# Optimization experiments

Measured on AMD Instinct MI355X. Metric: run time of the kernel, lower is better.

The kernel has to match this reference:

```python
import jax, jax.numpy as jnp
import numpy as np

D = 512          # token_dim * num_heads
TOKEN_DIM = 256
SCALE = TOKEN_DIM ** (-0.5)


def _l2norm(x, axis):
    # torch.nn.functional.normalize: x / max(||x||_2, eps)
    n = jnp.linalg.norm(x, axis=axis, keepdims=True)
    return x / jnp.maximum(n, 1e-12)


def setup_inputs() -> dict:
    key = jax.random.key(0)
    ks = jax.random.split(key, 32)
    B, N, IN = 8, 4096, 512
    s_in = 1.0 / np.sqrt(IN)
    s_d = 1.0 / np.sqrt(D)

    def lin(k, fin, fout, scale):
        kw, kb = jax.random.split(k)
        return (jax.random.uniform(kw, (fin, fout), jnp.float32, -scale, scale),
                jax.random.uniform(kb, (fout,), jnp.float32, -scale, scale))

    wq_I, bq_I = lin(ks[0], IN, D, s_in)
    wk_I, bk_I = lin(ks[1], IN, D, s_in)
    wq_M, bq_M = lin(ks[2], IN, D, s_in)
    wk_M, bk_M = lin(ks[3], IN, D, s_in)
    p1_w, p1_b = lin(ks[4], D, D, s_d)
    p2_w, p2_b = lin(ks[5], D, D, s_d)
    p3_w, p3_b = lin(ks[6], D, D, s_d)
    p4_w, p4_b = lin(ks[7], D, D, s_d)
    f_w, f_b = lin(ks[8], D, TOKEN_DIM, s_d)
    return {
        'x_I': jax.random.normal(ks[9], (B, N, IN), jnp.float32),
        'x_M': jax.random.normal(ks[10], (B, N, IN), jnp.float32),
        'wq_I': wq_I, 'bq_I': bq_I, 'wk_I': wk_I, 'bk_I': bk_I,
        'wq_M': wq_M, 'bq_M': bq_M, 'wk_M': wk_M, 'bk_M': bk_M,
        'wg_I': jax.random.normal(ks[11], (D, 1), jnp.float32),
        'wg_M': jax.random.normal(ks[12], (D, 1), jnp.float32),
        'p1_w': p1_w, 'p1_b': p1_b, 'p2_w': p2_w, 'p2_b': p2_b,
        'p3_w': p3_w, 'p3_b': p3_b, 'p4_w': p4_w, 'p4_b': p4_b,
        'f_w': f_w, 'f_b': f_b,
    }


def reference(x_I, x_M, wq_I, bq_I, wk_I, bk_I, wq_M, bq_M, wk_M, bk_M,
              wg_I, wg_M, p1_w, p1_b, p2_w, p2_b, p3_w, p3_b, p4_w, p4_b,
              f_w, f_b):
    # projections, then L2-normalize along feature dim
    q_I = _l2norm(x_I @ wq_I + bq_I, axis=-1)   # [B, N, D]
    k_I = _l2norm(x_I @ wk_I + bk_I, axis=-1)
    q_M = _l2norm(x_M @ wq_M + bq_M, axis=-1)
    k_M = _l2norm(x_M @ wk_M + bk_M, axis=-1)

    # softmax-free attention weights, L2-normalized over sequence dim
    A_I = _l2norm((q_I @ wg_I) * SCALE, axis=1)  # [B, N, 1]
    A_M = _l2norm((q_M @ wg_M) * SCALE, axis=1)

    # pooled global queries, broadcast back over tokens
    G_I = jnp.sum(A_I * q_I, axis=1, keepdims=True)  # [B, 1, D]
    G_M = jnp.sum(A_M * q_M, axis=1, keepdims=True)

    out = ((G_I * k_I) @ p1_w + p1_b
           + (G_I * k_M) @ p2_w + p2_b
           + (G_M * k_M) @ p3_w + p3_b
           + (G_M * k_I) @ p4_w + p4_b
           + q_I + q_M)                              # [B, N, D]
    return out @ f_w + f_b                           # [B, N, token_dim]
```

## Files before the change

kernel.cpp:

```cpp
#include <hip/hip_runtime.h>

typedef unsigned short u16;
typedef unsigned int   u32;
typedef __bf16 bf16_t;
typedef bf16_t bf16x8 __attribute__((ext_vector_type(8)));
typedef float  f32x4  __attribute__((ext_vector_type(4)));

__device__ __forceinline__ float b2f(u16 u){
  u32 x = ((u32)u) << 16;
  return __builtin_bit_cast(float, x);
}
__device__ __forceinline__ u16 f2b(float f){
  u32 u = __builtin_bit_cast(u32, f);
  u32 r = u + 0x7FFFu + ((u >> 16) & 1u);
  return (u16)(r >> 16);
}

union V8 { uint4 q; u16 u[8]; };

__device__ __forceinline__ void gld16(const u16* gsrc, u16* ldst){
  __builtin_amdgcn_global_load_lds(
      (const __attribute__((address_space(1))) u32*)gsrc,
      (__attribute__((address_space(3))) u32*)ldst, 16, 0, 0);
}

struct CArgs { const float* src[4]; u16* dst[4]; int cnt[4]; };

__global__ __launch_bounds__(256) void convert_k(CArgs c){
  int z = blockIdx.z;
  int i8 = (blockIdx.x * 256 + threadIdx.x) * 8;
  if (i8 >= c.cnt[z]) return;
  const float* s = c.src[z] + i8;
  float4 a = *(const float4*)s;
  float4 b = *(const float4*)(s + 4);
  V8 o;
  o.u[0]=f2b(a.x); o.u[1]=f2b(a.y); o.u[2]=f2b(a.z); o.u[3]=f2b(a.w);
  o.u[4]=f2b(b.x); o.u[5]=f2b(b.y); o.u[6]=f2b(b.z); o.u[7]=f2b(b.w);
  *(uint4*)(c.dst[z] + i8) = o.q;
}

struct TArgs { const float* src[5]; u16* dst[5]; int ncol[5]; };

__global__ __launch_bounds__(256) void transpose_k(TArgs t,
    const float* __restrict__ p1b, const float* __restrict__ p2b,
    const float* __restrict__ p3b, const float* __restrict__ p4b,
    const float* __restrict__ fw, const float* __restrict__ fb,
    float* __restrict__ cb, float* __restrict__ Gun)
{
  __shared__ u16 T[64][65];
  __shared__ float sb[512];
  int z = blockIdx.z;
  int tid = threadIdx.x;
  if (z == 5){
    if (blockIdx.x == 0 && blockIdx.y == 0){
      sb[tid]       = p1b[tid] + p2b[tid] + p3b[tid] + p4b[tid];
      sb[tid + 256] = p1b[tid+256] + p2b[tid+256] + p3b[tid+256] + p4b[tid+256];
      __syncthreads();
      float acc = 0.f;
      for (int j = 0; j < 512; j++) acc += sb[j] * fw[j*256 + tid];
      cb[tid] = acc + fb[tid];
    } else if (blockIdx.x >= 1 && blockIdx.x <= 4){
      int idx = ((blockIdx.x - 1)*8 + blockIdx.y)*256 + tid;
      Gun[idx] = 0.f;
    }
    return;
  }
  int nc = t.ncol[z];
  int j0 = blockIdx.y * 64;
  if (j0 >= nc) return;
  int i0 = blockIdx.x * 64;
  const float* s = t.src[z];
  u16* d = t.dst[z];
  #pragma unroll
  for (int rep = 0; rep < 16; rep++){
    int lin = rep*256 + tid;
    int r = lin >> 6, c = lin & 63;
    T[c][r] = f2b(s[(size_t)(i0 + r) * nc + j0 + c]);
  }
  __syncthreads();
  #pragma unroll
  for (int rep = 0; rep < 16; rep++){
    int lin = rep*256 + tid;
    int r = lin >> 6, c = lin & 63;
    d[(size_t)(j0 + r) * 512 + i0 + c] = T[r][c];
  }
}

__global__ __launch_bounds__(256, 2) void proj_k(
    const float* __restrict__ XI, const float* __restrict__ XM,
    const u16* __restrict__ WTI, const u16* __restrict__ WTM,
    const float* __restrict__ bqI, const float* __restrict__ bkI,
    const float* __restrict__ bqM, const float* __restrict__ bkM,
    const float* __restrict__ wgI, const float* __restrict__ wgM,
    u16* __restrict__ qI, u16* __restrict__ kI,
    u16* __restrict__ qM, u16* __restrict__ kM,
    float* __restrict__ Araw, float* __restrict__ Gun)
{
  const int tid = threadIdx.x, l = tid & 63, w = tid >> 6;
  const int m0 = blockIdx.x * 64;
  const int y  = blockIdx.y, zi = blockIdx.z;
  __shared__ __align__(16) u16 As[64*32];
  __shared__ __align__(16) u16 Bs[512*32];
  const int lr = l & 15, quad = l >> 4;
  const int srow = l >> 2, scol = (l & 3) * 8;
  const int wn = w * 128;

  const float* X  = zi ? XM : XI;
  const u16* Wbase = (zi ? WTM : WTI) + (size_t)y * 512 * 512;
  const float* bias = y ? (zi ? bkM : bkI) : (zi ? bqM : bqI);
  const float* wg   = zi ? wgM : wgI;
  u16* OUT = y ? (zi ? kM : kI) : (zi ? qM : qI);

  const int arow = w*16 + (l >> 2);
  const int aks  = (l & 3) * 8;

  f32x4 acc[4][8] = {};
  for (int k0 = 0; k0 < 512; k0 += 32){
    __syncthreads();
    {
      const float* src = X + (size_t)(m0 + arow)*512 + k0 + aks;
      float4 p0 = *(const float4*)src;
      float4 p1 = *(const float4*)(src + 4);
      V8 o;
      o.u[0]=f2b(p0.x); o.u[1]=f2b(p0.y); o.u[2]=f2b(p0.z); o.u[3]=f2b(p0.w);
      o.u[4]=f2b(p1.x); o.u[5]=f2b(p1.y); o.u[6]=f2b(p1.z); o.u[7]=f2b(p1.w);
      *(uint4*)&As[arow*32 + aks] = o.q;
    }
    #pragma unroll
    for (int i = 0; i < 8; i++)
      gld16(Wbase + (size_t)(wn + i*16 + srow)*512 + k0 + scol, &Bs[(w*8 + i)*512]);
    __syncthreads();
    bf16x8 aF[4], bF[8];
    #pragma unroll
    for (int mt = 0; mt < 4; mt++)
      aF[mt] = *(const bf16x8*)&As[(mt*16 + lr)*32 + quad*8];
    #pragma unroll
    for (int nt = 0; nt < 8; nt++)
      bF[nt] = *(const bf16x8*)&Bs[(wn + nt*16 + lr)*32 + quad*8];
    #pragma unroll
    for (int mt = 0; mt < 4; mt++){
      #pragma unroll
      for (int nt = 0; nt < 8; nt++)
        acc[mt][nt] = __builtin_amdgcn_mfma_f32_16x16x32_bf16(aF[mt], bF[nt], acc[mt][nt], 0, 0, 0);
    }
  }

  float wgv[8];
  if (y == 0){
    #pragma unroll
    for (int nt = 0; nt < 8; nt++) wgv[nt] = wg[wn + nt*16 + lr];
  }
  #pragma unroll
  for (int nt = 0; nt < 8; nt++){
    float bcol = bias[wn + nt*16 + lr];
    #pragma unroll
    for (int mt = 0; mt < 4; mt++)
      #pragma unroll
      for (int r = 0; r < 4; r++)
        acc[mt][nt][r] += bcol;
  }
  float ss[4][4], dq[4][4];
  #pragma unroll
  for (int mt = 0; mt < 4; mt++)
    #pragma unroll
    for (int r = 0; r < 4; r++){
      float s = 0.f, d = 0.f;
      #pragma unroll
      for (int nt = 0; nt < 8; nt++){
        float v = acc[mt][nt][r];
        s += v*v;
        if (y == 0) d += v * wgv[nt];
      }
      ss[mt][r] = s; dq[mt][r] = d;
    }
  #pragma unroll
  for (int off = 1; off < 16; off <<= 1){
    #pragma unroll
    for (int mt = 0; mt < 4; mt++)
      #pragma unroll
      for (int r = 0; r < 4; r++){
        ss[mt][r] += __shfl_xor(ss[mt][r], off, 64);
        if (y == 0) dq[mt][r] += __shfl_xor(dq[mt][r], off, 64);
      }
  }
  __syncthreads();
  float* red    = (float*)As;
  float* red2   = red + 256;
  float* rnS    = red2 + 256;
  float* araw_s = rnS + 64;
  if (lr == 0){
    #pragma unroll
    for (int mt = 0; mt < 4; mt++)
      #pragma unroll
      for (int r = 0; r < 4; r++){
        int row = mt*16 + quad*4 + r;
        red[w*64 + row] = ss[mt][r];
        if (y == 0) red2[w*64 + row] = dq[mt][r];
      }
  }
  __syncthreads();
  if (tid < 64){
    float t2 = red[tid] + red[64+tid] + red[128+tid] + red[192+tid];
    float rn = 1.f / fmaxf(sqrtf(t2), 1e-12f);
    rnS[tid] = rn;
    if (y == 0){
      float d = red2[tid] + red2[64+tid] + red2[128+tid] + red2[192+tid];
      float a = d * rn * 0.0625f;
      araw_s[tid] = a;
      Araw[zi*32768 + m0 + tid] = a;
    }
  }
  __syncthreads();
  float part[8] = {};
  #pragma unroll
  for (int mt = 0; mt < 4; mt++){
    f32x4 rn4 = *(const f32x4*)&rnS[mt*16 + quad*4];
    #pragma unroll
    for (int r = 0; r < 4; r++){
      float aw = (y == 0) ? araw_s[mt*16 + quad*4 + r] : 0.f;
      #pragma unroll
      for (int nt = 0; nt < 8; nt++){
        float v = acc[mt][nt][r] * rn4[r];
        OUT[(size_t)(m0 + mt*16 + quad*4 + r)*512 + wn + nt*16 + lr] = f2b(v);
        if (y == 0) part[nt] += aw * v;
      }
    }
  }
  if (y == 0){
    #pragma unroll
    for (int nt = 0; nt < 8; nt++){
      part[nt] += __shfl_xor(part[nt], 16, 64);
      part[nt] += __shfl_xor(part[nt], 32, 64);
    }
    if (quad == 0){
      int bb = blockIdx.x >> 6;
      #pragma unroll
      for (int nt = 0; nt < 8; nt++)
        atomicAdd(&Gun[((size_t)zi*8 + bb)*512 + wn + nt*16 + lr], part[nt]);
    }
  }
}

template<int MODE>
__global__ __launch_bounds__(256) void gemm2_k(
    const u16* __restrict__ A0, const u16* __restrict__ A1,
    const u16* __restrict__ A2, const u16* __restrict__ A3,
    const u16* __restrict__ BT,
    const float* __restrict__ cb,
    u16* __restrict__ Cq, float* __restrict__ Cf)
{
  constexpr int KTOT = (MODE == 2) ? 2048 : 512;
  const int tid = threadIdx.x, l = tid & 63, w = tid >> 6;
  const int m0 = blockIdx.x * 128, n0 = blockIdx.y * 128;
  __shared__ u16 As[128*32];
  __shared__ u16 Bs[128*32];
  f32x4 acc[4][4] = {};
  const int wm = (w >> 1) * 64, wn = (w & 1) * 64;
  const int lr = l & 15, quad = l >> 4;
  const int srow = l >> 2, scol = (l & 3) * 8;

  const u16* Bbase = BT;
  u16* Cqb = Cq;
  if constexpr (MODE == 2)
    Bbase = BT + (size_t)(m0 >> 12) * 256 * 2048;
  if constexpr (MODE == 1){
    Bbase = BT + (size_t)blockIdx.z * 262144;
    Cqb   = Cq + (size_t)blockIdx.z * 131072;
  }

  for (int k0 = 0; k0 < KTOT; k0 += 32){
    __syncthreads();
    const u16* Ab; int kloc;
    if constexpr (MODE == 2){
      int which = k0 >> 9; kloc = k0 & 511;
      Ab = (which == 0) ? A0 : (which == 1) ? A1 : (which == 2) ? A2 : A3;
    } else { Ab = A0; kloc = k0; }
    #pragma unroll
    for (int i = 0; i < 2; i++){
      int r = w*32 + i*16 + srow;
      gld16(Ab    + (size_t)(m0 + r) * 512  + kloc + scol, &As[(w*2 + i) * 512]);
      gld16(Bbase + (size_t)(n0 + r) * KTOT + k0   + scol, &Bs[(w*2 + i) * 512]);
    }
    __syncthreads();
    bf16x8 aF[4], bF[4];
    #pragma unroll
    for (int mt = 0; mt < 4; mt++)
      aF[mt] = *(const bf16x8*)&As[(wm + mt*16 + lr)*32 + quad*8];
    #pragma unroll
    for (int nt = 0; nt < 4; nt++)
      bF[nt] = *(const bf16x8*)&Bs[(wn + nt*16 + lr)*32 + quad*8];
    #pragma unroll
    for (int mt = 0; mt < 4; mt++){
      #pragma unroll
      for (int nt = 0; nt < 4; nt++)
        acc[mt][nt] = __builtin_amdgcn_mfma_f32_16x16x32_bf16(aF[mt], bF[nt], acc[mt][nt], 0, 0, 0);
    }
  }
  #pragma unroll
  for (int nt = 0; nt < 4; nt++){
    int col = n0 + wn + nt*16 + lr;
    #pragma unroll
    for (int mt = 0; mt < 4; mt++){
      int row0 = m0 + wm + mt*16 + quad*4;
      #pragma unroll
      for (int r = 0; r < 4; r++){
        int row = row0 + r;
        float v = acc[mt][nt][r];
        if constexpr (MODE == 1){
          Cqb[(size_t)row*512 + col] = f2b(v);
        } else {
          Cf[(size_t)row*256 + col] = v + cb[col];
        }
      }
    }
  }
}

__global__ __launch_bounds__(256) void ranorm_k(const float* __restrict__ Araw,
                                                float* __restrict__ rA){
  int idx = blockIdx.x;
  const float* A = Araw + idx*4096;
  int tid = threadIdx.x, l = tid & 63, w = tid >> 6;
  float ss = 0.f;
  for (int i = tid; i < 4096; i += 256){ float a = A[i]; ss += a*a; }
  #pragma unroll
  for (int off = 32; off > 0; off >>= 1) ss += __shfl_xor(ss, off, 64);
  __shared__ float red[4];
  if (l == 0) red[w] = ss;
  __syncthreads();
  if (tid == 0)
    rA[idx] = 1.f / fmaxf(sqrtf(red[0] + red[1] + red[2] + red[3]), 1e-12f);
}

__global__ __launch_bounds__(256) void weff_k(
    const u16* __restrict__ pfT, const u16* __restrict__ fT,
    const float* __restrict__ Gun, const float* __restrict__ rA,
    u16* __restrict__ WT)
{
  int b = blockIdx.x, o = blockIdx.y, tid = threadIdx.x;
  int k0 = tid * 8;
  V8 out;
  if (k0 < 1024){
    int kk = k0 & 511;
    const u16* pa = pfT + ((k0 < 512) ? 0      : 131072) + o*512 + kk;
    const u16* pb = pfT + ((k0 < 512) ? 393216 : 262144) + o*512 + kk;
    float rI = rA[b], rM = rA[8 + b];
    const float* gI = Gun + b*512 + kk;
    const float* gM = Gun + 4096 + b*512 + kk;
    V8 Pa, Pb; Pa.q = *(const uint4*)pa; Pb.q = *(const uint4*)pb;
    float4 gi0 = *(const float4*)gI, gi1 = *(const float4*)(gI+4);
    float4 gm0 = *(const float4*)gM, gm1 = *(const float4*)(gM+4);
    float gi[8] = {gi0.x,gi0.y,gi0.z,gi0.w,gi1.x,gi1.y,gi1.z,gi1.w};
    float gm[8] = {gm0.x,gm0.y,gm0.z,gm0.w,gm1.x,gm1.y,gm1.z,gm1.w};
    #pragma unroll
    for (int j = 0; j < 8; j++)
      out.u[j] = f2b(rI*gi[j]*b2f(Pa.u[j]) + rM*gm[j]*b2f(Pb.u[j]));
  } else {
    out.q = *(const uint4*)(fT + o*512 + (k0 & 511));
  }
  *(uint4*)(WT + ((size_t)b*256 + o)*2048 + k0) = out.q;
}

extern "C" void kernel_launch(void* const* d_in, const int* in_sizes, int n_in,
                              void* d_out, int out_size, void* d_ws, size_t ws_size,
                              hipStream_t stream)
{
  const float* x_I  = (const float*)d_in[0];
  const float* x_M  = (const float*)d_in[1];
  const float* wq_I = (const float*)d_in[2];
  const float* bq_I = (const float*)d_in[3];
  const float* wk_I = (const float*)d_in[4];
  const float* bk_I = (const float*)d_in[5];
  const float* wq_M = (const float*)d_in[6];
  const float* bq_M = (const float*)d_in[7];
  const float* wk_M = (const float*)d_in[8];
  const float* bk_M = (const float*)d_in[9];
  const float* wg_I = (const float*)d_in[10];
  const float* wg_M = (const float*)d_in[11];
  const float* p1_w = (const float*)d_in[12];
  const float* p1_b = (const float*)d_in[13];
  const float* p2_w = (const float*)d_in[14];
  const float* p2_b = (const float*)d_in[15];
  const float* p3_w = (const float*)d_in[16];
  const float* p3_b = (const float*)d_in[17];
  const float* p4_w = (const float*)d_in[18];
  const float* p4_b = (const float*)d_in[19];
  const float* f_w  = (const float*)d_in[20];
  const float* f_b  = (const float*)d_in[21];

  char* ws = (char*)d_ws;
  u16*  wqkT_I = (u16*)(ws + 0);
  u16*  wqkT_M = (u16*)(ws + 1048576);
  u16*  fT     = (u16*)(ws + 2097152);
  u16*  pcat   = (u16*)(ws + 2359296);
  u16*  pfT    = (u16*)(ws + 4456448);
  u16*  WT     = (u16*)(ws + 5505024);
  float* cb    = (float*)(ws + 13893632);
  float* Araw  = (float*)(ws + 13894656);
  float* rA    = (float*)(ws + 14156800);
  float* Gun   = (float*)(ws + 14157056);
  u16*  qIb    = (u16*)(ws + 14189824);
  u16*  kIb    = (u16*)(ws + 47744256);
  u16*  qMb    = (u16*)(ws + 81298688);
  u16*  kMb    = (u16*)(ws + 114853120);

  CArgs c;
  const float* csrc[4] = {p1_w, p2_w, p3_w, p4_w};
  u16* cdst[4] = {pcat, pcat + 262144, pcat + 524288, pcat + 786432};
  for (int i = 0; i < 4; i++){ c.src[i] = csrc[i]; c.dst[i] = cdst[i]; c.cnt[i] = 262144; }
  convert_k<<<dim3(128,1,4), 256, 0, stream>>>(c);

  TArgs t;
  const float* tsrc[5] = {wq_I, wk_I, wq_M, wk_M, f_w};
  u16* tdst[5] = {wqkT_I, wqkT_I + 262144, wqkT_M, wqkT_M + 262144, fT};
  int tnc[5] = {512, 512, 512, 512, 256};
  for (int i = 0; i < 5; i++){ t.src[i] = tsrc[i]; t.dst[i] = tdst[i]; t.ncol[i] = tnc[i]; }
  transpose_k<<<dim3(8,8,6), 256, 0, stream>>>(t, p1_b, p2_b, p3_b, p4_b, f_w, f_b, cb, Gun);

  gemm2_k<1><<<dim3(2,4,4), 256, 0, stream>>>(fT, nullptr, nullptr, nullptr,
      pcat, nullptr, pfT, nullptr);

  proj_k<<<dim3(512,2,2), 256, 0, stream>>>(x_I, x_M, wqkT_I, wqkT_M,
      bq_I, bk_I, bq_M, bk_M, wg_I, wg_M, qIb, kIb, qMb, kMb, Araw, Gun);

  ranorm_k<<<16, 256, 0, stream>>>(Araw, rA);

  weff_k<<<dim3(8,256), 256, 0, stream>>>(pfT, fT, Gun, rA, WT);

  gemm2_k<2><<<dim3(256,2), 256, 0, stream>>>(kIb, kMb, qIb, qMb,
      WT, cb, nullptr, (float*)d_out);
}
```

Baseline: 399.7 us.

## Double-buffer LDS tiles in projection and GEMM kernels to overlap loads

Both the projection kernel and the templated GEMM kernel now keep two LDS buffers for the A and B tiles. The loads for the next K-step are issued before the MFMA work on the current step, and only one barrier per iteration remains. In the projection kernel the fp32 activations are loaded early and converted to bf16 after the MFMAs, hiding global latency. This doubles LDS use: the projection kernel goes to about 72KB per block at a target of 2 blocks per CU, which may pressure occupancy and raise register use.

After: 392.2 us. Within noise of the previous version (-1.9%).

```diff
diff --git a/kernel.cpp b/kernel.cpp
--- a/kernel.cpp
+++ b/kernel.cpp
@@ -99,8 +99,8 @@
   const int tid = threadIdx.x, l = tid & 63, w = tid >> 6;
   const int m0 = blockIdx.x * 64;
   const int y  = blockIdx.y, zi = blockIdx.z;
-  __shared__ __align__(16) u16 As[64*32];
-  __shared__ __align__(16) u16 Bs[512*32];
+  __shared__ __align__(16) u16 As[2][64*32];
+  __shared__ __align__(16) u16 Bs[2][512*32];
   const int lr = l & 15, quad = l >> 4;
   const int srow = l >> 2, scol = (l & 3) * 8;
   const int wn = w * 128;
@@ -113,36 +113,56 @@
 
   const int arow = w*16 + (l >> 2);
   const int aks  = (l & 3) * 8;
+  const float* aptr = X + (size_t)(m0 + arow)*512 + aks;
 
   f32x4 acc[4][8] = {};
-  for (int k0 = 0; k0 < 512; k0 += 32){
-    __syncthreads();
-    {
-      const float* src = X + (size_t)(m0 + arow)*512 + k0 + aks;
-      float4 p0 = *(const float4*)src;
-      float4 p1 = *(const float4*)(src + 4);
+
+  {
+    float4 p0 = *(const float4*)(aptr);
+    float4 p1 = *(const float4*)(aptr + 4);
+    V8 o;
+    o.u[0]=f2b(p0.x); o.u[1]=f2b(p0.y); o.u[2]=f2b(p0.z); o.u[3]=f2b(p0.w);
+    o.u[4]=f2b(p1.x); o.u[5]=f2b(p1.y); o.u[6]=f2b(p1.z); o.u[7]=f2b(p1.w);
+    *(uint4*)&As[0][arow*32 + aks] = o.q;
+    #pragma unroll
+    for (int i = 0; i < 8; i++)
+      gld16(Wbase + (size_t)(wn + i*16 + srow)*512 + scol, &Bs[0][(w*8 + i)*512]);
+  }
+  __syncthreads();
+
+  #pragma unroll
+  for (int kk = 0; kk < 16; kk++){
+    const int k0 = kk * 32;
+    const int cur = kk & 1, nxt = cur ^ 1;
+    const int kn = k0 + 32;
+    float4 p0, p1;
+    if (kn < 512){
+      #pragma unroll
+      for (int i = 0; i < 8; i++)
+        gld16(Wbase + (size_t)(wn + i*16 + srow)*512 + kn + scol, &Bs[nxt][(w*8 + i)*512]);
+      p0 = *(const float4*)(aptr + kn);
+      p1 = *(const float4*)(aptr + kn + 4);
+    }
+    bf16x8 aF[4], bF[8];
+    #pragma unroll
+    for (int mt = 0; mt < 4; mt++)
+      aF[mt] = *(const bf16x8*)&As[cur][(mt*16 + lr)*32 + quad*8];
+    #pragma unroll
+    for (int nt = 0; nt < 8; nt++)
+      bF[nt] = *(const bf16x8*)&Bs[cur][(wn + nt*16 + lr)*32 + quad*8];
+    #pragma unroll
+    for (int mt = 0; mt < 4; mt++){
+      #pragma unroll
+      for (int nt = 0; nt < 8; nt++)
+        acc[mt][nt] = __builtin_amdgcn_mfma_f32_16x16x32_bf16(aF[mt], bF[nt], acc[mt][nt], 0, 0, 0);
+    }
+    if (kn < 512){
       V8 o;
       o.u[0]=f2b(p0.x); o.u[1]=f2b(p0.y); o.u[2]=f2b(p0.z); o.u[3]=f2b(p0.w);
       o.u[4]=f2b(p1.x); o.u[5]=f2b(p1.y); o.u[6]=f2b(p1.z); o.u[7]=f2b(p1.w);
-      *(uint4*)&As[arow*32 + aks] = o.q;
-    }
-    #pragma unroll
-    for (int i = 0; i < 8; i++)
-      gld16(Wbase + (size_t)(wn + i*16 + srow)*512 + k0 + scol, &Bs[(w*8 + i)*512]);
+      *(uint4*)&As[nxt][arow*32 + aks] = o.q;
+    }
     __syncthreads();
-    bf16x8 aF[4], bF[8];
-    #pragma unroll
-    for (int mt = 0; mt < 4; mt++)
-      aF[mt] = *(const bf16x8*)&As[(mt*16 + lr)*32 + quad*8];
-    #pragma unroll
-    for (int nt = 0; nt < 8; nt++)
-      bF[nt] = *(const bf16x8*)&Bs[(wn + nt*16 + lr)*32 + quad*8];
-    #pragma unroll
-    for (int mt = 0; mt < 4; mt++){
-      #pragma unroll
-      for (int nt = 0; nt < 8; nt++)
-        acc[mt][nt] = __builtin_amdgcn_mfma_f32_16x16x32_bf16(aF[mt], bF[nt], acc[mt][nt], 0, 0, 0);
-    }
   }
 
   float wgv[8];
@@ -252,8 +272,8 @@
   constexpr int KTOT = (MODE == 2) ? 2048 : 512;
   const int tid = threadIdx.x, l = tid & 63, w = tid >> 6;
   const int m0 = blockIdx.x * 128, n0 = blockIdx.y * 128;
-  __shared__ u16 As[128*32];
-  __shared__ u16 Bs[128*32];
+  __shared__ u16 As[2][128*32];
+  __shared__ u16 Bs[2][128*32];
   f32x4 acc[4][4] = {};
   const int wm = (w >> 1) * 64, wn = (w & 1) * 64;
   const int lr = l & 15, quad = l >> 4;
@@ -268,34 +288,47 @@
     Cqb   = Cq + (size_t)blockIdx.z * 131072;
   }
 
+  #pragma unroll
+  for (int i = 0; i < 2; i++){
+    int r = w*32 + i*16 + srow;
+    gld16(A0    + (size_t)(m0 + r) * 512  + scol, &As[0][(w*2 + i) * 512]);
+    gld16(Bbase + (size_t)(n0 + r) * KTOT + scol, &Bs[0][(w*2 + i) * 512]);
+  }
+  __syncthreads();
+
+  #pragma unroll 2
   for (int k0 = 0; k0 < KTOT; k0 += 32){
-    __syncthreads();
-    const u16* Ab; int kloc;
-    if constexpr (MODE == 2){
-      int which = k0 >> 9; kloc = k0 & 511;
-      Ab = (which == 0) ? A0 : (which == 1) ? A1 : (which == 2) ? A2 : A3;
-    } else { Ab = A0; kloc = k0; }
-    #pragma unroll
-    for (int i = 0; i < 2; i++){
-      int r = w*32 + i*16 + srow;
-      gld16(Ab    + (size_t)(m0 + r) * 512  + kloc + scol, &As[(w*2 + i) * 512]);
-      gld16(Bbase + (size_t)(n0 + r) * KTOT + k0   + scol, &Bs[(w*2 + i) * 512]);
-    }
-    __syncthreads();
+    const int cur = (k0 >> 5) & 1, nxt = cur ^ 1;
+    const int kn = k0 + 32;
+    if (kn < KTOT){
+      const u16* Ab; int kloc;
+      if constexpr (MODE == 2){
+        int which = kn >> 9; kloc = kn & 511;
+        Ab = (which == 0) ? A0 : (which == 1) ? A1 : (which == 2) ? A2 : A3;
+      } else { Ab = A0; kloc = kn; }
+      #pragma unroll
+      for (int i = 0; i < 2; i++){
+        int r = w*32 + i*16 + srow;
+        gld16(Ab    + (size_t)(m0 + r) * 512  + kloc + scol, &As[nxt][(w*2 + i) * 512]);
+        gld16(Bbase + (size_t)(n0 + r) * KTOT + kn   + scol, &Bs[nxt][(w*2 + i) * 512]);
+      }
+    }
     bf16x8 aF[4], bF[4];
     #pragma unroll
     for (int mt = 0; mt < 4; mt++)
-      aF[mt] = *(const bf16x8*)&As[(wm + mt*16 + lr)*32 + quad*8];
+      aF[mt] = *(const bf16x8*)&As[cur][(wm + mt*16 + lr)*32 + quad*8];
     #pragma unroll
     for (int nt = 0; nt < 4; nt++)
-      bF[nt] = *(const bf16x8*)&Bs[(wn + nt*16 + lr)*32 + quad*8];
+      bF[nt] = *(const bf16x8*)&Bs[cur][(wn + nt*16 + lr)*32 + quad*8];
     #pragma unroll
     for (int mt = 0; mt < 4; mt++){
       #pragma unroll
       for (int nt = 0; nt < 4; nt++)
         acc[mt][nt] = __builtin_amdgcn_mfma_f32_16x16x32_bf16(aF[mt], bF[nt], acc[mt][nt], 0, 0, 0);
     }
-  }
+    __syncthreads();
+  }
+
   #pragma unroll
   for (int nt = 0; nt < 4; nt++){
     int col = n0 + wn + nt*16 + lr;
```

## Software-pipeline projection and second-stage GEMMs with multi-buffered LDS prefetch

Applied to the files above, without the earlier changes.

The projection kernel now double-buffers both the bf16-converted activation tile and the weight tile. Global loads for the next K-step are issued before the MFMAs of the current step, and the previous two syncthreads per iteration become a single barrier guarded by explicit vmcnt waits. The second GEMM kernel gets a 4-deep LDS ring with three stages in flight, setprio around the MFMA block, and launch bounds of 2 blocks per SM. This is meant to hide global-load latency behind compute, at the cost of more LDS per block, which may limit occupancy. The hand-written waitcnt and barrier sequencing also makes correctness fragile.

New measurement: 386.4 us. 1.03x faster.

```diff
diff --git a/kernel.cpp b/kernel.cpp
--- a/kernel.cpp
+++ b/kernel.cpp
@@ -99,51 +99,105 @@
   const int tid = threadIdx.x, l = tid & 63, w = tid >> 6;
   const int m0 = blockIdx.x * 64;
   const int y  = blockIdx.y, zi = blockIdx.z;
-  __shared__ __align__(16) u16 As[64*32];
-  __shared__ __align__(16) u16 Bs[512*32];
+  __shared__ __align__(16) u16 As[2][64*32];
+  __shared__ __align__(16) u16 Bs[2][4][4096];
   const int lr = l & 15, quad = l >> 4;
   const int srow = l >> 2, scol = (l & 3) * 8;
   const int wn = w * 128;
 
   const float* X  = zi ? XM : XI;
-  const u16* Wbase = (zi ? WTM : WTI) + (size_t)y * 512 * 512;
+  const u16* Wbase = (zi ? WTM : WTI) + (size_t)y * 512 * 512 + (size_t)wn * 512;
   const float* bias = y ? (zi ? bkM : bkI) : (zi ? bqM : bqI);
   const float* wg   = zi ? wgM : wgI;
   u16* OUT = y ? (zi ? kM : kI) : (zi ? qM : qI);
 
   const int arow = w*16 + (l >> 2);
   const int aks  = (l & 3) * 8;
+  const float* aptr = X + (size_t)(m0 + arow)*512 + aks;
 
   f32x4 acc[4][8] = {};
-  for (int k0 = 0; k0 < 512; k0 += 32){
-    __syncthreads();
-    {
-      const float* src = X + (size_t)(m0 + arow)*512 + k0 + aks;
-      float4 p0 = *(const float4*)src;
-      float4 p1 = *(const float4*)(src + 4);
-      V8 o;
-      o.u[0]=f2b(p0.x); o.u[1]=f2b(p0.y); o.u[2]=f2b(p0.z); o.u[3]=f2b(p0.w);
-      o.u[4]=f2b(p1.x); o.u[5]=f2b(p1.y); o.u[6]=f2b(p1.z); o.u[7]=f2b(p1.w);
-      *(uint4*)&As[arow*32 + aks] = o.q;
-    }
-    #pragma unroll
-    for (int i = 0; i < 8; i++)
-      gld16(Wbase + (size_t)(wn + i*16 + srow)*512 + k0 + scol, &Bs[(w*8 + i)*512]);
-    __syncthreads();
+  float4 s0a, s0b, s1a, s1b;
+
+  s0a = *(const float4*)(aptr);
+  s0b = *(const float4*)(aptr + 4);
+  __builtin_amdgcn_sched_barrier(0);
+  #pragma unroll
+  for (int i = 0; i < 8; i++)
+    gld16(Wbase + (size_t)(i*16 + srow)*512 + scol, &Bs[0][w][i*512]);
+  __builtin_amdgcn_sched_barrier(0);
+  s1a = *(const float4*)(aptr + 32);
+  s1b = *(const float4*)(aptr + 36);
+  __builtin_amdgcn_sched_barrier(0);
+  {
+    V8 o;
+    o.u[0]=f2b(s0a.x); o.u[1]=f2b(s0a.y); o.u[2]=f2b(s0a.z); o.u[3]=f2b(s0a.w);
+    o.u[4]=f2b(s0b.x); o.u[5]=f2b(s0b.y); o.u[6]=f2b(s0b.z); o.u[7]=f2b(s0b.w);
+    *(uint4*)&As[0][arow*32 + aks] = o.q;
+  }
+  asm volatile("s_waitcnt vmcnt(2)" ::: "memory");
+  asm volatile("s_waitcnt lgkmcnt(0)" ::: "memory");
+  __builtin_amdgcn_sched_barrier(0);
+  __builtin_amdgcn_s_barrier();
+
+#define PBODY(P, CV0, CV1, LD0, LD1, KA, KB, DOLOAD, VMC) do{                              \
+    bf16x8 aF[4], bF[8];                                                                   \
+    _Pragma("unroll")                                                                      \
+    for (int mt = 0; mt < 4; mt++)                                                         \
+      aF[mt] = *(const bf16x8*)&As[(P)][(mt*16 + lr)*32 + quad*8];                         \
+    _Pragma("unroll")                                                                      \
+    for (int nt = 0; nt < 8; nt++)                                                         \
+      bF[nt] = *(const bf16x8*)&Bs[(P)][w][(nt*16 + lr)*32 + quad*8];                      \
+    __builtin_amdgcn_sched_barrier(0);                                                     \
+    _Pragma("unroll")                                                                      \
+    for (int i = 0; i < 8; i++)                                                            \
+      gld16(Wbase + (size_t)(i*16 + srow)*512 + (KB) + scol, &Bs[(P)^1][w][i*512]);        \
+    __builtin_amdgcn_sched_barrier(0);                                                     \
+    if (DOLOAD){                                                                           \
+      LD0 = *(const float4*)(aptr + (KA));                                                 \
+      LD1 = *(const float4*)(aptr + (KA) + 4);                                             \
+    }                                                                                      \
+    __builtin_amdgcn_sched_barrier(0);                                                     \
+    { V8 o;                                                                                \
+      o.u[0]=f2b((CV0).x); o.u[1]=f2b((CV0).y); o.u[2]=f2b((CV0).z); o.u[3]=f2b((CV0).w); \
+      o.u[4]=f2b((CV1).x); o.u[5]=f2b((CV1).y); o.u[6]=f2b((CV1).z); o.u[7]=f2b((CV1).w); \
+      *(uint4*)&As[(P)^1][arow*32 + aks] = o.q; }                                          \
+    __builtin_amdgcn_s_setprio(1);                                                         \
+    _Pragma("unroll")                                                                      \
+    for (int mt = 0; mt < 4; mt++){                                                        \
+      _Pragma("unroll")                                                                    \
+      for (int nt = 0; nt < 8; nt++)                                                       \
+        acc[mt][nt] = __builtin_amdgcn_mfma_f32_16x16x32_bf16(aF[mt], bF[nt], acc[mt][nt], 0, 0, 0); \
+    }                                                                                      \
+    __builtin_amdgcn_s_setprio(0);                                                         \
+    asm volatile("s_waitcnt vmcnt(" #VMC ")" ::: "memory");                                \
+    asm volatile("s_waitcnt lgkmcnt(0)" ::: "memory");                                     \
+    __builtin_amdgcn_sched_barrier(0);                                                     \
+    __builtin_amdgcn_s_barrier();                                                          \
+  } while(0)
+
+  for (int tt = 0; tt < 7; ++tt){
+    PBODY(0, s1a, s1b, s0a, s0b, (2*tt+2)*32, (2*tt+1)*32, 1, 2);
+    PBODY(1, s0a, s0b, s1a, s1b, (2*tt+3)*32, (2*tt+2)*32, 1, 2);
+  }
+  PBODY(0, s1a, s1b, s0a, s0b, 0, 480, 0, 0);
+  {
     bf16x8 aF[4], bF[8];
     #pragma unroll
     for (int mt = 0; mt < 4; mt++)
-      aF[mt] = *(const bf16x8*)&As[(mt*16 + lr)*32 + quad*8];
+      aF[mt] = *(const bf16x8*)&As[1][(mt*16 + lr)*32 + quad*8];
     #pragma unroll
     for (int nt = 0; nt < 8; nt++)
-      bF[nt] = *(const bf16x8*)&Bs[(wn + nt*16 + lr)*32 + quad*8];
+      bF[nt] = *(const bf16x8*)&Bs[1][w][(nt*16 + lr)*32 + quad*8];
+    __builtin_amdgcn_s_setprio(1);
     #pragma unroll
     for (int mt = 0; mt < 4; mt++){
       #pragma unroll
       for (int nt = 0; nt < 8; nt++)
         acc[mt][nt] = __builtin_amdgcn_mfma_f32_16x16x32_bf16(aF[mt], bF[nt], acc[mt][nt], 0, 0, 0);
     }
-  }
+    __builtin_amdgcn_s_setprio(0);
+  }
+#undef PBODY
 
   float wgv[8];
   if (y == 0){
@@ -242,7 +296,7 @@
 }
 
 template<int MODE>
-__global__ __launch_bounds__(256) void gemm2_k(
+__global__ __launch_bounds__(256, 2) void gemm2_k(
     const u16* __restrict__ A0, const u16* __restrict__ A1,
     const u16* __restrict__ A2, const u16* __restrict__ A3,
     const u16* __restrict__ BT,
@@ -250,10 +304,10 @@
     u16* __restrict__ Cq, float* __restrict__ Cf)
 {
   constexpr int KTOT = (MODE == 2) ? 2048 : 512;
+  constexpr int NT   = KTOT / 32;
   const int tid = threadIdx.x, l = tid & 63, w = tid >> 6;
   const int m0 = blockIdx.x * 128, n0 = blockIdx.y * 128;
-  __shared__ u16 As[128*32];
-  __shared__ u16 Bs[128*32];
+  __shared__ __align__(16) u16 S[4][2][4096];
   f32x4 acc[4][4] = {};
   const int wm = (w >> 1) * 64, wn = (w & 1) * 64;
   const int lr = l & 15, quad = l >> 4;
@@ -268,34 +322,56 @@
     Cqb   = Cq + (size_t)blockIdx.z * 131072;
   }
 
-  for (int k0 = 0; k0 < KTOT; k0 += 32){
-    __syncthreads();
+  auto stage = [&](int kk, int buf) __attribute__((always_inline)) {
     const u16* Ab; int kloc;
     if constexpr (MODE == 2){
-      int which = k0 >> 9; kloc = k0 & 511;
+      int which = kk >> 9; kloc = kk & 511;
       Ab = (which == 0) ? A0 : (which == 1) ? A1 : (which == 2) ? A2 : A3;
-    } else { Ab = A0; kloc = k0; }
+    } else { Ab = A0; kloc = kk; }
     #pragma unroll
     for (int i = 0; i < 2; i++){
       int r = w*32 + i*16 + srow;
-      gld16(Ab    + (size_t)(m0 + r) * 512  + kloc + scol, &As[(w*2 + i) * 512]);
-      gld16(Bbase + (size_t)(n0 + r) * KTOT + k0   + scol, &Bs[(w*2 + i) * 512]);
-    }
-    __syncthreads();
+      gld16(Ab    + (size_t)(m0 + r) * 512  + kloc + scol, &S[buf][0][(w*2 + i)*512]);
+      gld16(Bbase + (size_t)(n0 + r) * KTOT + kk   + scol, &S[buf][1][(w*2 + i)*512]);
+    }
+  };
+
+  stage(0, 0);
+  stage(32, 1);
+  stage(64, 2);
+  asm volatile("s_waitcnt vmcnt(8)" ::: "memory");
+  __builtin_amdgcn_sched_barrier(0);
+  __builtin_amdgcn_s_barrier();
+
+  for (int t = 0; t < NT; ++t){
+    const u16* Sc = &S[t & 3][0][0];
     bf16x8 aF[4], bF[4];
     #pragma unroll
     for (int mt = 0; mt < 4; mt++)
-      aF[mt] = *(const bf16x8*)&As[(wm + mt*16 + lr)*32 + quad*8];
+      aF[mt] = *(const bf16x8*)&Sc[(wm + mt*16 + lr)*32 + quad*8];
     #pragma unroll
     for (int nt = 0; nt < 4; nt++)
-      bF[nt] = *(const bf16x8*)&Bs[(wn + nt*16 + lr)*32 + quad*8];
+      bF[nt] = *(const bf16x8*)&Sc[4096 + (wn + nt*16 + lr)*32 + quad*8];
+    if (t < NT - 1){
+      int kn = (t + 3 < NT) ? (t + 3)*32 : 0;
+      stage(kn, (t + 3) & 3);
+    }
+    __builtin_amdgcn_s_setprio(1);
     #pragma unroll
     for (int mt = 0; mt < 4; mt++){
       #pragma unroll
       for (int nt = 0; nt < 4; nt++)
         acc[mt][nt] = __builtin_amdgcn_mfma_f32_16x16x32_bf16(aF[mt], bF[nt], acc[mt][nt], 0, 0, 0);
     }
-  }
+    __builtin_amdgcn_s_setprio(0);
+    if (t < NT - 1){
+      asm volatile("s_waitcnt vmcnt(8)" ::: "memory");
+      __builtin_amdgcn_sched_barrier(0);
+      __builtin_amdgcn_s_barrier();
+    }
+  }
+  asm volatile("s_waitcnt vmcnt(0)" ::: "memory");
+
   #pragma unroll
   for (int nt = 0; nt < 4; nt++){
     int col = n0 + wn + nt*16 + lr;
```
